# Kernel optimization log

Measured on AMD Instinct MI355X. Metric: run time of the kernel, lower is better.

The kernel has to match this reference:

```python
import jax, jax.numpy as jnp
import numpy as np

B, S, H, N, D = 2, 2048, 1024, 16, 64  # batch, seq, hidden, heads, head_size
PAD = -30000.0


def setup_inputs() -> dict:
    key = jax.random.key(0)
    kx, kqkv, kout, krpe = jax.random.split(key, 4)
    x = jax.random.normal(kx, (B, S, H), jnp.float32)
    qkv = jax.random.normal(kqkv, (H, 3, N, D), jnp.float32) * H ** (-0.5)
    out_w = jax.random.normal(kout, (N, D, H), jnp.float32) * (N * D) ** (-0.5)
    # rpe_bias is zero-init in torch; use small randn so the bias path is exercised
    rpe_bias = jax.random.normal(krpe, (N, S), jnp.float32) * 0.02
    return {"x": x, "qkv": qkv, "out_w": out_w, "rpe_bias": rpe_bias}


def reference(x, qkv, out_w, rpe_bias):
    # q, k, v: [B, N, S, D]
    q, k, v = jnp.einsum('bsx,xMnd->Mbnsd', x, qkv)
    s = x.shape[1]
    a = jnp.einsum('bnsd,bntd->bnst', q, k) * q.shape[-1] ** (-0.5)
    # cumulative relative-position bias: bias[n, i, j] = cumsum(rpe)[n, i-j] for i>=j,
    # PAD otherwise (exactly what to_tril produces on the row-broadcast cumsum).
    cum = jnp.cumsum(rpe_bias[:, :s], axis=-1)            # [N, S]
    rel = jnp.arange(s)[:, None] - jnp.arange(s)[None, :]  # [S, S], i - j
    bias = jnp.where(rel >= 0, cum[:, jnp.clip(rel, 0)], PAD)  # [N, S, S]
    a = jax.nn.softmax(a + bias, axis=-1)
    mix = jnp.einsum('bnst,bntd->bnsd', a, v)
    return jnp.einsum('bnsd,ndx->bsx', mix, out_w)
```

## Files before the change

### kernel.cpp

```cpp
#include <hip/hip_runtime.h>
#include <hip/hip_bf16.h>
#include <cstdint>
#include <cstddef>

#define B_   2
#define S_   2048
#define H_   1024
#define NH   16
#define DH   64
#define LOG2E 1.4426950408889634f
#define SCALE2 (0.125f * LOG2E)

typedef __hip_bfloat16 bf16;
typedef short bf16x8 __attribute__((ext_vector_type(8)));
typedef float f32x4 __attribute__((ext_vector_type(4)));

#define MFMA16(a, b, c) __builtin_amdgcn_mfma_f32_16x16x32_bf16((a), (b), (c), 0, 0, 0)

__device__ __forceinline__ void async16(const void* g, void* l) {
  __builtin_amdgcn_global_load_lds(
      (const __attribute__((address_space(1))) void*)g,
      (__attribute__((address_space(3))) void*)l,
      16, 0, 0);
}
__device__ __forceinline__ void async4(const void* g, void* l) {
  __builtin_amdgcn_global_load_lds(
      (const __attribute__((address_space(1))) void*)g,
      (__attribute__((address_space(3))) void*)l,
      4, 0, 0);
}

__device__ __forceinline__ void tr_body(const float* __restrict__ src,
                                        bf16* __restrict__ dst, int R, int C,
                                        int c0, int r0, bf16 (*tile)[33], int tid) {
  int tx = tid & 31, ty = tid >> 5;
  for (int i = 0; i < 32; i += 8)
    tile[ty + i][tx] = __float2bfloat16(src[(size_t)(r0 + ty + i) * C + c0 + tx]);
  __syncthreads();
  for (int i = 0; i < 32; i += 8)
    dst[(size_t)(c0 + ty + i) * R + r0 + tx] = tile[tx][ty + i];
}

__global__ __launch_bounds__(256)
void prep(const float* __restrict__ x, bf16* __restrict__ xb,
          const float* __restrict__ qkv, bf16* __restrict__ qkvT,
          const float* __restrict__ outw, bf16* __restrict__ outwT,
          const float* __restrict__ rpe, float* __restrict__ cum) {
  __shared__ char pm[2176] __attribute__((aligned(16)));
  const int L = blockIdx.x, tid = threadIdx.x;
  if (L < 4096) {
    int i = (L * 256 + tid) * 4;
    float4 v = *(const float4*)(x + i);
    bf16 o[4] = {__float2bfloat16(v.x), __float2bfloat16(v.y),
                 __float2bfloat16(v.z), __float2bfloat16(v.w)};
    *(uint64_t*)(xb + i) = *(const uint64_t*)o;
  } else if (L < 7168) {
    int t = L - 4096;
    int cx = t % 96, ry = t / 96;
    tr_body(qkv, qkvT, 1024, 3072, cx * 32, ry * 32, (bf16(*)[33])pm, tid);
  } else if (L < 8192) {
    int t = L - 7168;
    int cx = t & 31, ry = t >> 5;
    tr_body(outw, outwT, 1024, 1024, cx * 32, ry * 32, (bf16(*)[33])pm, tid);
  } else {
    float* ssum = (float*)pm;
    int n = L - 8192;
    float loc[8];
    float s = 0.f;
    int base = tid * 8;
#pragma unroll
    for (int u = 0; u < 8; ++u) {
      loc[u] = rpe[n * S_ + base + u];
      s += loc[u];
    }
    ssum[tid] = s;
    __syncthreads();
    float own = s;
    for (int off = 1; off < 256; off <<= 1) {
      float v = (tid >= off) ? ssum[tid - off] : 0.f;
      __syncthreads();
      ssum[tid] += v;
      __syncthreads();
    }
    float run = ssum[tid] - own;
#pragma unroll
    for (int u = 0; u < 8; ++u) {
      run += loc[u];
      cum[n * S_ + base + u] = run * LOG2E;
    }
  }
}

template <int MODE>
__global__ __launch_bounds__(256, MODE == 0 ? 3 : 2)
void gemm_bt(const bf16* __restrict__ A, const bf16* __restrict__ Bt,
             bf16* __restrict__ C0, bf16* __restrict__ C1, bf16* __restrict__ C2,
             float* __restrict__ F0) {
  constexpr int NT = (MODE == 0) ? 4 : 2;
  constexpr int NB = NT * 32;
  __shared__ char smem[MODE == 0 ? 36864 : 12288] __attribute__((aligned(16)));
  bf16* As = (bf16*)smem;
  bf16* Bs = (bf16*)(smem + 8192);
  const int tid = threadIdx.x, lane = tid & 63, w = tid >> 6;
  const int lr = lane & 15, lq = lane >> 4;
  const int m0 = blockIdx.y * 128, n0 = blockIdx.x * NB;
  const int wm = (w & 1) * 64, wn = (w >> 1) * (NT * 16);

  f32x4 acc[4][NT] = {};

  for (int k0 = 0; k0 < 1024; k0 += 32) {
    __syncthreads();
#pragma unroll
    for (int t = 0; t < 2; ++t) {
      int c = (t * 4 + w) * 64 + lane;
      int row = c >> 2, ch = c & 3;
      int k8 = (ch ^ ((row >> 1) & 3)) * 8;
      async16(A + (size_t)(m0 + row) * 1024 + k0 + k8,
              (char*)As + (size_t)(t * 4 + w) * 1024 + lane * 16);
    }
#pragma unroll
    for (int t = 0; t < NB / 64; ++t) {
      int c = (t * 4 + w) * 64 + lane;
      int row = c >> 2, ch = c & 3;
      int k8 = (ch ^ ((row >> 1) & 3)) * 8;
      async16(Bt + (size_t)(n0 + row) * 1024 + k0 + k8,
              (char*)Bs + (size_t)(t * 4 + w) * 1024 + lane * 16);
    }
    __syncthreads();
    bf16x8 af[4], bfr[NT];
#pragma unroll
    for (int mt = 0; mt < 4; ++mt) {
      int row = wm + mt * 16 + lr;
      af[mt] = *(const bf16x8*)(As + row * 32 + ((lq ^ ((row >> 1) & 3)) << 3));
    }
#pragma unroll
    for (int nt = 0; nt < NT; ++nt) {
      int row = wn + nt * 16 + lr;
      bfr[nt] = *(const bf16x8*)(Bs + row * 32 + ((lq ^ ((row >> 1) & 3)) << 3));
    }
#pragma unroll
    for (int mt = 0; mt < 4; ++mt)
#pragma unroll
      for (int nt = 0; nt < NT; ++nt)
        acc[mt][nt] = MFMA16(af[mt], bfr[nt], acc[mt][nt]);
  }

  if (MODE == 0) {
    __syncthreads();
    bf16* E = (bf16*)smem + w * (64 * 72);
    const int cbase = n0 + wn;
    const int mm = cbase >> 10, nn = (cbase >> 6) & 15;
    const int bb = (m0 + wm) >> 11;
    const int sbase = (m0 + wm) & 2047;
    if (mm < 2) {
#pragma unroll
      for (int mt = 0; mt < 4; ++mt)
#pragma unroll
        for (int nt = 0; nt < 4; ++nt)
#pragma unroll
          for (int r = 0; r < 4; ++r)
            E[(mt * 16 + lq * 4 + r) * 72 + nt * 16 + lr] =
                __float2bfloat16(acc[mt][nt][r]);
      bf16* dst = (mm == 0 ? C0 : C1) +
                  ((size_t)(bb * NH + nn) * S_ + sbase) * DH;
#pragma unroll
      for (int it = 0; it < 8; ++it) {
        int c = it * 64 + lane;
        int rw = c >> 3, c8 = c & 7;
        *(uint4*)(dst + (size_t)rw * DH + c8 * 8) =
            *(const uint4*)(E + rw * 72 + c8 * 8);
      }
    } else {
#pragma unroll
      for (int mt = 0; mt < 4; ++mt)
#pragma unroll
        for (int nt = 0; nt < 4; ++nt)
#pragma unroll
          for (int r = 0; r < 4; ++r)
            E[(nt * 16 + lr) * 72 + mt * 16 + lq * 4 + r] =
                __float2bfloat16(acc[mt][nt][r]);
      bf16* dst = C2 + (size_t)(bb * NH + nn) * DH * S_;
#pragma unroll
      for (int it = 0; it < 8; ++it) {
        int c = it * 64 + lane;
        int dr = c >> 3, c8 = c & 7;
        *(uint4*)(dst + (size_t)dr * S_ + sbase + c8 * 8) =
            *(const uint4*)(E + dr * 72 + c8 * 8);
      }
    }
  } else {
#pragma unroll
    for (int mt = 0; mt < 4; ++mt)
#pragma unroll
      for (int nt = 0; nt < NT; ++nt)
#pragma unroll
        for (int r = 0; r < 4; ++r) {
          int rM = m0 + wm + mt * 16 + lq * 4 + r;
          int cN = n0 + wn + nt * 16 + lr;
          F0[(size_t)rM * 1024 + cN] = acc[mt][nt][r];
        }
  }
}

__device__ __forceinline__ void fa_stage(const bf16* __restrict__ k,
                                         const bf16* __restrict__ vt,
                                         const float* __restrict__ cumn,
                                         char* smem, int bn, int i0, int j0,
                                         int buf, int tid) {
  char* dst = smem + buf * 16384;
  const char* ksrc = (const char*)(k + ((size_t)bn * S_ + j0) * DH);
#pragma unroll
  for (int t = 0; t < 2; ++t) {
    int c = t * 256 + tid;
    int row = c >> 3, ch = c & 7;
    int cs = ch ^ (row & 7);
    async16(ksrc + row * 128 + cs * 16, dst + c * 16);
  }
  const char* vsrc = (const char*)(vt + (size_t)bn * DH * S_);
#pragma unroll
  for (int t = 0; t < 2; ++t) {
    int c = t * 256 + tid;
    int row = c >> 3, ch = c & 7;
    int cs = ch ^ (row & 7);
    async16(vsrc + (size_t)row * (S_ * 2) + j0 * 2 + cs * 16,
            dst + 8192 + c * 16);
  }
  float* cdst = (float*)(smem + 51200) + buf * 1056;
  int base = i0 - j0 - 63 + tid;
#pragma unroll
  for (int p = 0; p < 4; ++p) {
    int src = base + p;
    src = src < 0 ? 0 : (src > S_ - 1 ? S_ - 1 : src);
    async4(cumn + src, cdst + p * 264 + tid);
  }
}

__global__ __launch_bounds__(256, 2)
void fa_kernel(const bf16* __restrict__ q, const bf16* __restrict__ k,
               const bf16* __restrict__ vt, const float* __restrict__ cum,
               bf16* __restrict__ mix) {
  __shared__ char smem[59648] __attribute__((aligned(16)));
  bf16* Ps = (bf16*)(smem + 32768);

  const int tid = threadIdx.x, lane = tid & 63, w = tid >> 6;
  const int lr = lane & 15, lq = lane >> 4;

  const int L = blockIdx.x;
  const int half = L >> 8;
  const int idx = L & 255;
  const int xcd = idx & 7, slot = idx >> 3;
  const int bn = xcd + 8 * (slot & 3);
  const int pr = slot >> 2;
  const int ti = half ? pr : (15 - pr);
  const int n = bn & (NH - 1);
  const int b = bn >> 4;
  const float* cumn = cum + n * S_;

  const int i0 = ti << 7;
  const int NI = 2 * ti + 2;

  const bf16* qbase = q + ((size_t)bn * S_ + i0 + w * 32) * DH;
  bf16x8 qf[2][2];
#pragma unroll
  for (int is = 0; is < 2; ++is)
#pragma unroll
    for (int kt = 0; kt < 2; ++kt)
      qf[is][kt] = *(const bf16x8*)(qbase + (is * 16 + lr) * DH + kt * 32 + lq * 8);

  bf16x8 ones;
#pragma unroll
  for (int u = 0; u < 8; ++u) ones[u] = (short)0x3F80;

  f32x4 oacc[2][4] = {};
  f32x4 lacc[2] = {};

  fa_stage(k, vt, cumn, smem, bn, i0, 0, 0, tid);

  for (int g = 0; g < NI; ++g) {
    const int bsel = g & 1;
    const char* kb = smem + bsel * 16384;
    const char* vb = kb + 8192;
    const float* cumB = (const float*)(smem + 51200) + bsel * 1056;
    const int j0 = g << 6;
    const int doff = i0 - j0;

    __syncthreads();

    if (g + 1 < NI)
      fa_stage(k, vt, cumn, smem, bn, i0, (g + 1) << 6, bsel ^ 1, tid);

    f32x4 sa[2][4] = {};
#pragma unroll
    for (int kt = 0; kt < 2; ++kt)
#pragma unroll
      for (int nt = 0; nt < 4; ++nt) {
        int krow = nt * 16 + lr;
        bf16x8 kf = *(const bf16x8*)(kb + krow * 128 +
                        (((kt * 4 + lq) ^ (krow & 7)) << 4));
        sa[0][nt] = MFMA16(kf, qf[0][kt], sa[0][nt]);
        sa[1][nt] = MFMA16(kf, qf[1][kt], sa[1][nt]);
      }

#pragma unroll
    for (int is = 0; is < 2; ++is) {
      const int ilocI = w * 32 + is * 16 + lr;
      if (doff >= 64) {
#pragma unroll
        for (int nt = 0; nt < 4; ++nt) {
          int jl = nt * 16 + lq * 4;
          int Xm3 = 60 + ilocI - jl;
          int p = Xm3 & 3, b0 = Xm3 & ~3;
          f32x4 cv = *(const f32x4*)(cumB + p * 264 + b0);
          bf16 pk[4];
#pragma unroll
          for (int r = 0; r < 4; ++r)
            pk[r] = __float2bfloat16(exp2f(sa[is][nt][r] * SCALE2 + cv[3 - r]));
          *(uint64_t*)(Ps + ilocI * 72 + nt * 16 + lq * 4) = *(const uint64_t*)pk;
        }
      } else {
#pragma unroll
        for (int nt = 0; nt < 4; ++nt) {
          int jl = nt * 16 + lq * 4;
          int Xm3 = 60 + ilocI - jl;
          int p = Xm3 & 3, b0 = Xm3 & ~3;
          f32x4 cv = *(const f32x4*)(cumB + p * 264 + b0);
          bf16 pk[4];
#pragma unroll
          for (int r = 0; r < 4; ++r) {
            float pv = (doff + ilocI - jl - r >= 0)
                           ? exp2f(sa[is][nt][r] * SCALE2 + cv[3 - r])
                           : 0.f;
            pk[r] = __float2bfloat16(pv);
          }
          *(uint64_t*)(Ps + ilocI * 72 + nt * 16 + lq * 4) = *(const uint64_t*)pk;
        }
      }
    }

#pragma unroll
    for (int kt2 = 0; kt2 < 2; ++kt2) {
      bf16x8 pf0 = *(const bf16x8*)(Ps + (w * 32 + lr) * 72 + kt2 * 32 + lq * 8);
      bf16x8 pf1 = *(const bf16x8*)(Ps + (w * 32 + 16 + lr) * 72 + kt2 * 32 + lq * 8);
      lacc[0] = MFMA16(pf0, ones, lacc[0]);
      lacc[1] = MFMA16(pf1, ones, lacc[1]);
#pragma unroll
      for (int dt = 0; dt < 4; ++dt) {
        int vrow = dt * 16 + lr;
        bf16x8 vf = *(const bf16x8*)(vb + vrow * 128 +
                        (((kt2 * 4 + lq) ^ (vrow & 7)) << 4));
        oacc[0][dt] = MFMA16(pf0, vf, oacc[0][dt]);
        oacc[1][dt] = MFMA16(pf1, vf, oacc[1][dt]);
      }
    }
  }

#pragma unroll
  for (int is = 0; is < 2; ++is)
#pragma unroll
    for (int dt = 0; dt < 4; ++dt)
#pragma unroll
      for (int r = 0; r < 4; ++r) {
        int i = i0 + w * 32 + is * 16 + lq * 4 + r;
        int d = dt * 16 + lr;
        mix[((size_t)(b * S_ + i) * NH + n) * DH + d] =
            __float2bfloat16(oacc[is][dt][r] / lacc[is][r]);
      }
}

extern "C" void kernel_launch(void* const* d_in, const int* in_sizes, int n_in,
                              void* d_out, int out_size, void* d_ws, size_t ws_size,
                              hipStream_t stream) {
  const float* x     = (const float*)d_in[0];
  const float* qkv   = (const float*)d_in[1];
  const float* out_w = (const float*)d_in[2];
  const float* rpe   = (const float*)d_in[3];
  float* out = (float*)d_out;

  char* ws = (char*)d_ws;
  bf16* qkvT  = (bf16*)(ws + 0);
  bf16* outwT = (bf16*)(ws + 6291456);
  bf16* xb    = (bf16*)(ws + 8388608);
  bf16* qb    = (bf16*)(ws + 16777216);
  bf16* kb    = (bf16*)(ws + 25165824);
  bf16* vtb   = (bf16*)(ws + 33554432);
  bf16* mixb  = (bf16*)(ws + 41943040);
  float* cum  = (float*)(ws + 50331648);

  prep<<<8208, 256, 0, stream>>>(x, xb, qkv, qkvT, out_w, outwT, rpe, cum);
  gemm_bt<0><<<dim3(3072 / 128, 4096 / 128), 256, 0, stream>>>(xb, qkvT, qb, kb, vtb, nullptr);
  fa_kernel<<<512, 256, 0, stream>>>(qb, kb, vtb, cum, mixb);
  gemm_bt<1><<<dim3(1024 / 64, 4096 / 128), 256, 0, stream>>>(mixb, outwT, nullptr, nullptr, nullptr, out);
}
```

Measured before the change: 194.0 us.

## Split attention key tiles across waves with 64-row query tiles and paired scheduling

The attention kernel moves from 128-row query tiles, where each wave owned 32 rows, to 64-row query tiles. Each of two wave pairs handles half of every 64-key tile, and the two partial O/l accumulators are merged through shared memory at the diagonal tile. Each block processes a long and a short query tile back to back (T0=31-pp and T1=pp), so every block does exactly 33 iterations for balanced causal work. The smaller cumulative-bias staging shrinks LDS use, which may raise occupancy. The cost is extra syncs and a shared-memory reduction at each tile's end.

```diff
diff --git a/kernel.cpp b/kernel.cpp
--- a/kernel.cpp
+++ b/kernel.cpp
@@ -225,13 +225,15 @@
     async16(vsrc + (size_t)row * (S_ * 2) + j0 * 2 + cs * 16,
             dst + 8192 + c * 16);
   }
-  float* cdst = (float*)(smem + 51200) + buf * 1056;
-  int base = i0 - j0 - 63 + tid;
-#pragma unroll
-  for (int p = 0; p < 4; ++p) {
-    int src = base + p;
-    src = src < 0 ? 0 : (src > S_ - 1 ? S_ - 1 : src);
-    async4(cumn + src, cdst + p * 264 + tid);
+  if (tid < 136) {
+    float* cdst = (float*)(smem + 41984) + buf * 544;
+    int base = i0 - j0 - 63 + tid;
+#pragma unroll
+    for (int p = 0; p < 4; ++p) {
+      int src = base + p;
+      src = src < 0 ? 0 : (src > S_ - 1 ? S_ - 1 : src);
+      async4(cumn + src, cdst + p * 136 + tid);
+    }
   }
 }
 
@@ -239,91 +241,105 @@
 void fa_kernel(const bf16* __restrict__ q, const bf16* __restrict__ k,
                const bf16* __restrict__ vt, const float* __restrict__ cum,
                bf16* __restrict__ mix) {
-  __shared__ char smem[59648] __attribute__((aligned(16)));
+  __shared__ char smem[46592] __attribute__((aligned(16)));
   bf16* Ps = (bf16*)(smem + 32768);
+  float* combL = (float*)(smem + 46336);
 
   const int tid = threadIdx.x, lane = tid & 63, w = tid >> 6;
   const int lr = lane & 15, lq = lane >> 4;
+  const int rg = w & 1, jh = w >> 1;
 
   const int L = blockIdx.x;
-  const int half = L >> 8;
-  const int idx = L & 255;
-  const int xcd = idx & 7, slot = idx >> 3;
+  const int xcd = L & 7, slot = L >> 3;
   const int bn = xcd + 8 * (slot & 3);
-  const int pr = slot >> 2;
-  const int ti = half ? pr : (15 - pr);
+  const int pp = slot >> 2;
   const int n = bn & (NH - 1);
   const int b = bn >> 4;
   const float* cumn = cum + n * S_;
 
-  const int i0 = ti << 7;
-  const int NI = 2 * ti + 2;
-
-  const bf16* qbase = q + ((size_t)bn * S_ + i0 + w * 32) * DH;
+  const int T0 = 31 - pp;
+  const int T1 = pp;
+  const int nu0 = T0 + 1;
+
+  bf16x8 ones;
+#pragma unroll
+  for (int u = 0; u < 8; ++u) ones[u] = (short)0x3F80;
+  const f32x4 fz = {0.f, 0.f, 0.f, 0.f};
+
   bf16x8 qf[2][2];
-#pragma unroll
-  for (int is = 0; is < 2; ++is)
-#pragma unroll
-    for (int kt = 0; kt < 2; ++kt)
-      qf[is][kt] = *(const bf16x8*)(qbase + (is * 16 + lr) * DH + kt * 32 + lq * 8);
-
-  bf16x8 ones;
-#pragma unroll
-  for (int u = 0; u < 8; ++u) ones[u] = (short)0x3F80;
-
-  f32x4 oacc[2][4] = {};
-  f32x4 lacc[2] = {};
-
-  fa_stage(k, vt, cumn, smem, bn, i0, 0, 0, tid);
-
-  for (int g = 0; g < NI; ++g) {
+  f32x4 oacc[2][4];
+  f32x4 lacc[2];
+
+  fa_stage(k, vt, cumn, smem, bn, T0 * 64, 0, 0, tid);
+
+  int ti = T0, jt = 0, i0 = T0 * 64;
+
+  for (int g = 0; g < 33; ++g) {
     const int bsel = g & 1;
     const char* kb = smem + bsel * 16384;
     const char* vb = kb + 8192;
-    const float* cumB = (const float*)(smem + 51200) + bsel * 1056;
-    const int j0 = g << 6;
-    const int doff = i0 - j0;
+    const float* cumB = (const float*)(smem + 41984) + bsel * 544;
+    const int j0 = jt * 64;
+    const bool diag = (jt == ti);
 
     __syncthreads();
 
-    if (g + 1 < NI)
-      fa_stage(k, vt, cumn, smem, bn, i0, (g + 1) << 6, bsel ^ 1, tid);
-
-    f32x4 sa[2][4] = {};
+    if (g + 1 < 33) {
+      int gn = g + 1, tin, jtn;
+      if (gn < nu0) { tin = T0; jtn = gn; }
+      else          { tin = T1; jtn = gn - nu0; }
+      fa_stage(k, vt, cumn, smem, bn, tin * 64, jtn * 64, bsel ^ 1, tid);
+    }
+
+    if (jt == 0) {
+      const bf16* qbase = q + ((size_t)bn * S_ + i0 + rg * 32) * DH;
+#pragma unroll
+      for (int is = 0; is < 2; ++is) {
+#pragma unroll
+        for (int kt = 0; kt < 2; ++kt)
+          qf[is][kt] = *(const bf16x8*)(qbase + (is * 16 + lr) * DH + kt * 32 + lq * 8);
+        lacc[is] = fz;
+#pragma unroll
+        for (int dt = 0; dt < 4; ++dt) oacc[is][dt] = fz;
+      }
+    }
+
+    f32x4 sa[2][2] = {};
 #pragma unroll
     for (int kt = 0; kt < 2; ++kt)
 #pragma unroll
-      for (int nt = 0; nt < 4; ++nt) {
-        int krow = nt * 16 + lr;
+      for (int nt = 0; nt < 2; ++nt) {
+        int krow = jh * 32 + nt * 16 + lr;
         bf16x8 kf = *(const bf16x8*)(kb + krow * 128 +
                         (((kt * 4 + lq) ^ (krow & 7)) << 4));
         sa[0][nt] = MFMA16(kf, qf[0][kt], sa[0][nt]);
         sa[1][nt] = MFMA16(kf, qf[1][kt], sa[1][nt]);
       }
 
+    const int doff = i0 - j0;
 #pragma unroll
     for (int is = 0; is < 2; ++is) {
-      const int ilocI = w * 32 + is * 16 + lr;
-      if (doff >= 64) {
-#pragma unroll
-        for (int nt = 0; nt < 4; ++nt) {
-          int jl = nt * 16 + lq * 4;
+      const int ilocI = rg * 32 + is * 16 + lr;
+      if (!diag) {
+#pragma unroll
+        for (int nt = 0; nt < 2; ++nt) {
+          int jl = jh * 32 + nt * 16 + lq * 4;
           int Xm3 = 60 + ilocI - jl;
-          int p = Xm3 & 3, b0 = Xm3 & ~3;
-          f32x4 cv = *(const f32x4*)(cumB + p * 264 + b0);
+          int ph = Xm3 & 3, b0 = Xm3 & ~3;
+          f32x4 cv = *(const f32x4*)(cumB + ph * 136 + b0);
           bf16 pk[4];
 #pragma unroll
           for (int r = 0; r < 4; ++r)
             pk[r] = __float2bfloat16(exp2f(sa[is][nt][r] * SCALE2 + cv[3 - r]));
-          *(uint64_t*)(Ps + ilocI * 72 + nt * 16 + lq * 4) = *(const uint64_t*)pk;
+          *(uint64_t*)(Ps + ilocI * 72 + jl) = *(const uint64_t*)pk;
         }
       } else {
 #pragma unroll
-        for (int nt = 0; nt < 4; ++nt) {
-          int jl = nt * 16 + lq * 4;
+        for (int nt = 0; nt < 2; ++nt) {
+          int jl = jh * 32 + nt * 16 + lq * 4;
           int Xm3 = 60 + ilocI - jl;
-          int p = Xm3 & 3, b0 = Xm3 & ~3;
-          f32x4 cv = *(const f32x4*)(cumB + p * 264 + b0);
+          int ph = Xm3 & 3, b0 = Xm3 & ~3;
+          f32x4 cv = *(const f32x4*)(cumB + ph * 136 + b0);
           bf16 pk[4];
 #pragma unroll
           for (int r = 0; r < 4; ++r) {
@@ -332,39 +348,79 @@
                            : 0.f;
             pk[r] = __float2bfloat16(pv);
           }
-          *(uint64_t*)(Ps + ilocI * 72 + nt * 16 + lq * 4) = *(const uint64_t*)pk;
+          *(uint64_t*)(Ps + ilocI * 72 + jl) = *(const uint64_t*)pk;
         }
       }
     }
 
-#pragma unroll
-    for (int kt2 = 0; kt2 < 2; ++kt2) {
-      bf16x8 pf0 = *(const bf16x8*)(Ps + (w * 32 + lr) * 72 + kt2 * 32 + lq * 8);
-      bf16x8 pf1 = *(const bf16x8*)(Ps + (w * 32 + 16 + lr) * 72 + kt2 * 32 + lq * 8);
+    {
+      bf16x8 pf0 = *(const bf16x8*)(Ps + (rg * 32 + lr) * 72 + jh * 32 + lq * 8);
+      bf16x8 pf1 = *(const bf16x8*)(Ps + (rg * 32 + 16 + lr) * 72 + jh * 32 + lq * 8);
       lacc[0] = MFMA16(pf0, ones, lacc[0]);
       lacc[1] = MFMA16(pf1, ones, lacc[1]);
 #pragma unroll
       for (int dt = 0; dt < 4; ++dt) {
         int vrow = dt * 16 + lr;
         bf16x8 vf = *(const bf16x8*)(vb + vrow * 128 +
-                        (((kt2 * 4 + lq) ^ (vrow & 7)) << 4));
+                        (((jh * 4 + lq) ^ (vrow & 7)) << 4));
         oacc[0][dt] = MFMA16(pf0, vf, oacc[0][dt]);
         oacc[1][dt] = MFMA16(pf1, vf, oacc[1][dt]);
       }
     }
-  }
-
-#pragma unroll
-  for (int is = 0; is < 2; ++is)
-#pragma unroll
-    for (int dt = 0; dt < 4; ++dt)
-#pragma unroll
-      for (int r = 0; r < 4; ++r) {
-        int i = i0 + w * 32 + is * 16 + lq * 4 + r;
-        int d = dt * 16 + lr;
-        mix[((size_t)(b * S_ + i) * NH + n) * DH + d] =
-            __float2bfloat16(oacc[is][dt][r] / lacc[is][r]);
-      }
+
+    if (diag) {
+      __syncthreads();
+      float* scr = (float*)(smem + bsel * 16384) + rg * 2048;
+      if (jh == 1) {
+#pragma unroll
+        for (int is = 0; is < 2; ++is) {
+#pragma unroll
+          for (int dt = 0; dt < 4; ++dt)
+#pragma unroll
+            for (int r = 0; r < 4; ++r) {
+              int row = is * 16 + lq * 4 + r;
+              int col = ((dt ^ lq) << 4) + lr;
+              scr[row * 64 + col] = oacc[is][dt][r];
+            }
+          if (lr == 0)
+#pragma unroll
+            for (int r = 0; r < 4; ++r)
+              combL[rg * 32 + is * 16 + lq * 4 + r] = lacc[is][r];
+        }
+      }
+      __syncthreads();
+      if (jh == 0) {
+#pragma unroll
+        for (int is = 0; is < 2; ++is) {
+#pragma unroll
+          for (int r = 0; r < 4; ++r)
+            lacc[is][r] += combL[rg * 32 + is * 16 + lq * 4 + r];
+#pragma unroll
+          for (int dt = 0; dt < 4; ++dt)
+#pragma unroll
+            for (int r = 0; r < 4; ++r) {
+              int row = is * 16 + lq * 4 + r;
+              int col = ((dt ^ lq) << 4) + lr;
+              oacc[is][dt][r] += scr[row * 64 + col];
+            }
+        }
+#pragma unroll
+        for (int is = 0; is < 2; ++is)
+#pragma unroll
+          for (int dt = 0; dt < 4; ++dt)
+#pragma unroll
+            for (int r = 0; r < 4; ++r) {
+              int i = i0 + rg * 32 + is * 16 + lq * 4 + r;
+              int d = dt * 16 + lr;
+              mix[((size_t)(b * S_ + i) * NH + n) * DH + d] =
+                  __float2bfloat16(oacc[is][dt][r] / lacc[is][r]);
+            }
+      }
+      ti = T1; jt = 0; i0 = T1 * 64;
+    } else {
+      ++jt;
+    }
+  }
 }
 
 extern "C" void kernel_launch(void* const* d_in, const int* in_sizes, int n_in,
```

Measured after the change: 184.8 us. -4.7%, faster.
